# Kernel tuning notes

Measured on AMD Instinct MI355X. Metric: run time of the kernel, lower is better.

The kernel has to match this reference:

```python
import jax, jax.numpy as jnp
import numpy as np

B, IN, K, E = 2048, 1024, 128, 64  # batch, in_features, n_concepts, emb_size


def setup_inputs() -> dict:
    key = jax.random.key(0)
    k1, k2, k3, k4, k5 = jax.random.split(key, 5)
    x = jax.random.normal(k1, (B, IN), dtype=jnp.float32)
    # stacked per-concept Linear(in_features, 2*emb_size)
    W = jax.random.normal(k2, (K, IN, 2 * E), dtype=jnp.float32) * (1.0 / np.sqrt(IN))
    b = jax.random.normal(k3, (K, 2 * E), dtype=jnp.float32) * 0.01
    # shared prob predictor Linear(2*emb_size, 1)
    wp = jax.random.normal(k4, (2 * E,), dtype=jnp.float32) * (1.0 / np.sqrt(2 * E))
    bp = jax.random.normal(k5, (), dtype=jnp.float32) * 0.01
    return {"x": x, "W": W, "b": b, "wp": wp, "bp": bp}


def reference(x, W, b, wp, bp):
    # batched GEMM over all concepts at once: [B,K,2E]
    context = jax.nn.leaky_relu(jnp.einsum('bi,kio->bko', x, W) + b)
    # shared predictor + sigmoid: [B,K]
    c_pred = jax.nn.sigmoid(jnp.einsum('bko,o->bk', context, wp) + bp)
    ctx_pos = context[..., :E]
    ctx_neg = context[..., E:]
    p = c_pred[..., None]
    c_emb = ctx_pos * p + ctx_neg * (1.0 - p)  # [B,K,E]
    return c_emb, c_pred
```

## Files before the change

kernel.cpp:

```cpp
#include <hip/hip_runtime.h>

typedef unsigned int u32;
typedef unsigned short u16;
typedef __attribute__((ext_vector_type(8))) __bf16 bf16x8;
typedef __attribute__((ext_vector_type(4))) float f32x4;

#define B_SZ 2048
#define IN_SZ 1024
#define K_SZ 128
#define E_SZ 64
#define TWOE 128
#define BK 32
static const size_t OUT_EMB = (size_t)B_SZ * K_SZ * E_SZ;

__device__ __forceinline__ u16 f2bf(float f) {
    u32 u = __builtin_bit_cast(u32, f);
    u32 r = u + 0x7fffu + ((u >> 16) & 1u);
    return (u16)(r >> 16);
}

__device__ __forceinline__ void async16(const void* g, void* l) {
    __builtin_amdgcn_global_load_lds((const __attribute__((address_space(1))) u32*)g,
                                     (__attribute__((address_space(3))) u32*)l, 16, 0, 0);
}

__global__ void __launch_bounds__(256) cvt_x(const float* __restrict__ in, u16* __restrict__ outp, int n4) {
    int i = blockIdx.x * blockDim.x + threadIdx.x;
    if (i < n4) {
        float4 v = ((const float4*)in)[i];
        u32 lo = (u32)f2bf(v.x) | ((u32)f2bf(v.y) << 16);
        u32 hi = (u32)f2bf(v.z) | ((u32)f2bf(v.w) << 16);
        ((uint2*)outp)[i] = make_uint2(lo, hi);
    }
}

__global__ void __launch_bounds__(256) cvt_w(const float* __restrict__ W, u16* __restrict__ wt) {
    __shared__ u16 tr[128][72];
    const int k = blockIdx.y, i0 = blockIdx.x * 64;
    const float* src = W + (size_t)k * IN_SZ * TWOE + (size_t)i0 * TWOE;
#pragma unroll
    for (int r = 0; r < 8; ++r) {
        int idx = r * 256 + threadIdx.x;
        int i = idx >> 5;
        int o = (idx & 31) * 4;
        float4 v = ((const float4*)src)[idx];
        tr[o + 0][i] = f2bf(v.x);
        tr[o + 1][i] = f2bf(v.y);
        tr[o + 2][i] = f2bf(v.z);
        tr[o + 3][i] = f2bf(v.w);
    }
    __syncthreads();
    const int o = threadIdx.x >> 1, h = threadIdx.x & 1;
    u16* dst = wt + ((size_t)(k * TWOE + o) * IN_SZ) + i0 + h * 32;
#pragma unroll
    for (int s = 0; s < 4; ++s) {
        uint4 v = *(const uint4*)&tr[o][h * 32 + s * 8];
        ((uint4*)dst)[s] = v;
    }
}

__global__ void __launch_bounds__(256) cvt_pred(const float* __restrict__ pw, float* __restrict__ out) {
    __shared__ float t[128][132];
    const int b0 = blockIdx.x * 128;
    const int tid = threadIdx.x;
#pragma unroll
    for (int i = 0; i < 16; ++i) {
        int idx = i * 256 + tid;
        int kk = idx >> 5, c4 = (idx & 31) * 4;
        float4 v = *(const float4*)(pw + (size_t)kk * B_SZ + b0 + c4);
        t[kk][c4 + 0] = v.x; t[kk][c4 + 1] = v.y; t[kk][c4 + 2] = v.z; t[kk][c4 + 3] = v.w;
    }
    __syncthreads();
#pragma unroll
    for (int i = 0; i < 16; ++i) {
        int idx = i * 256 + tid;
        int bl = idx >> 5, k4 = (idx & 31) * 4;
        float4 v = make_float4(t[k4 + 0][bl], t[k4 + 1][bl], t[k4 + 2][bl], t[k4 + 3][bl]);
        *(float4*)(out + OUT_EMB + (size_t)(b0 + bl) * K_SZ + k4) = v;
    }
}

__global__ void __launch_bounds__(512, 2) fused_main(
    const u16* __restrict__ xb,
    const u16* __restrict__ wt,
    const float* __restrict__ bias, const float* __restrict__ wpv,
    const float* __restrict__ bpp, float* __restrict__ out,
    float* __restrict__ pw) {
    __shared__ union {
        u16 stage[3][20480];
        struct { float pl[512][2]; float ex[256][65]; } epi;
    } sm;

    const int tid = threadIdx.x;
    const int l = tid & 63, w = tid >> 6;
    const int wm = w >> 1, wn = w & 1;
    const int hi = l >> 4, lo16 = l & 15;
    const int q = l >> 2, sl = l & 3;

    const int id = blockIdx.x;
    const int xcd = id & 7, j = id >> 3;
    const int k = (xcd << 4) | (j >> 2);
    const int brow = (j & 3) << 9;

    const u16* abase = xb + (size_t)(brow + w * 16 + q) * IN_SZ + (sl ^ ((q >> 1) & 3)) * 8;
    const u16* bbase = wt + ((size_t)k * TWOE + w * 16 + q) * IN_SZ + (sl ^ ((q >> 1) & 3)) * 8;
    const int aldst = w * 512;
    const int bldst = 16384 + w * 512;

    const int xsl = (hi ^ ((lo16 >> 1) & 3)) << 4;
    const int aoff = (wm * 128 + lo16) * 64 + xsl;
    const int boff = 32768 + (wn * 64 + lo16) * 64 + xsl;

    f32x4 acc[8][4] = {};

    auto STAGE = [&](int bi, int tt) {
        const int koff = tt * BK;
        u16* sbuf = &sm.stage[bi][0];
#pragma unroll
        for (int i = 0; i < 4; ++i)
            async16(abase + (size_t)i * 128 * IN_SZ + koff, sbuf + i * 4096 + aldst);
        async16(bbase + koff, sbuf + bldst);
    };

    const float bp_val = *bpp;
    float bvals[4], wvals[4];
#pragma unroll
    for (int n = 0; n < 4; ++n) {
        const int o = wn * 64 + n * 16 + lo16;
        bvals[n] = bias[k * TWOE + o];
        wvals[n] = wpv[o];
    }

    STAGE(0, 0);
    STAGE(1, 1);
    asm volatile("s_waitcnt vmcnt(5)" ::: "memory");
    __builtin_amdgcn_s_barrier();

    for (int t = 0; t < 32; ++t) {
        const int b0 = t % 3;
        if (t < 30) STAGE((b0 + 2) % 3, t + 2);
        const char* base = (const char*)&sm.stage[b0][0];
        bf16x8 af[8], bfr[4];
#pragma unroll
        for (int m = 0; m < 8; ++m)
            af[m] = *(const bf16x8*)(base + aoff + m * 1024);
#pragma unroll
        for (int n = 0; n < 4; ++n)
            bfr[n] = *(const bf16x8*)(base + boff + n * 1024);
#pragma unroll
        for (int m = 0; m < 8; ++m)
#pragma unroll
            for (int n = 0; n < 4; ++n)
                acc[m][n] = __builtin_amdgcn_mfma_f32_16x16x32_bf16(af[m], bfr[n], acc[m][n], 0, 0, 0);
        if (t < 30) asm volatile("s_waitcnt vmcnt(5) lgkmcnt(0)" ::: "memory");
        else        asm volatile("s_waitcnt vmcnt(0) lgkmcnt(0)" ::: "memory");
        __builtin_amdgcn_s_barrier();
    }

    float p[8][4];
#pragma unroll
    for (int m = 0; m < 8; ++m)
#pragma unroll
        for (int j = 0; j < 4; ++j) {
            float s = 0.f;
#pragma unroll
            for (int n = 0; n < 4; ++n) {
                float v = acc[m][n][j] + bvals[n];
                v = v > 0.f ? v : 0.01f * v;
                acc[m][n][j] = v;
                s += v * wvals[n];
            }
            s += __shfl_xor(s, 1);
            s += __shfl_xor(s, 2);
            s += __shfl_xor(s, 4);
            s += __shfl_xor(s, 8);
            p[m][j] = s;
        }
    if (lo16 == 0) {
#pragma unroll
        for (int m = 0; m < 8; ++m)
#pragma unroll
            for (int j = 0; j < 4; ++j)
                sm.epi.pl[wm * 128 + m * 16 + hi * 4 + j][wn] = p[m][j];
    }
    __builtin_amdgcn_s_barrier();
#pragma unroll
    for (int m = 0; m < 8; ++m)
#pragma unroll
        for (int j = 0; j < 4; ++j) {
            const int rg = wm * 128 + m * 16 + hi * 4 + j;
            const float z = sm.epi.pl[rg][0] + sm.epi.pl[rg][1] + bp_val;
            p[m][j] = 1.f / (1.f + __expf(-z));
        }
    if (wn == 0 && lo16 == 0) {
        if (pw) {
#pragma unroll
            for (int m = 0; m < 8; ++m) {
                float4 v = make_float4(p[m][0], p[m][1], p[m][2], p[m][3]);
                *(float4*)(pw + (size_t)k * B_SZ + brow + wm * 128 + m * 16 + hi * 4) = v;
            }
        } else {
#pragma unroll
            for (int m = 0; m < 8; ++m)
#pragma unroll
                for (int j = 0; j < 4; ++j) {
                    const int b = brow + wm * 128 + m * 16 + hi * 4 + j;
                    out[OUT_EMB + (size_t)b * K_SZ + k] = p[m][j];
                }
        }
    }
#pragma unroll
    for (int h = 0; h < 2; ++h) {
        if (wn == 1) {
#pragma unroll
            for (int mm = 0; mm < 4; ++mm) {
                const int m = h * 4 + mm;
#pragma unroll
                for (int n = 0; n < 4; ++n)
#pragma unroll
                    for (int j = 0; j < 4; ++j)
                        sm.epi.ex[wm * 64 + mm * 16 + hi * 4 + j][n * 16 + lo16] =
                            (1.f - p[m][j]) * acc[m][n][j];
            }
        }
        __builtin_amdgcn_s_barrier();
        if (wn == 0) {
#pragma unroll
            for (int mm = 0; mm < 4; ++mm) {
                const int m = h * 4 + mm;
#pragma unroll
                for (int n = 0; n < 4; ++n)
#pragma unroll
                    for (int j = 0; j < 4; ++j) {
                        const int rl = wm * 64 + mm * 16 + hi * 4 + j;
                        const int b = brow + wm * 128 + m * 16 + hi * 4 + j;
                        const int e = n * 16 + lo16;
                        out[((size_t)b * K_SZ + k) * E_SZ + e] =
                            p[m][j] * acc[m][n][j] + sm.epi.ex[rl][e];
                    }
            }
        }
        __builtin_amdgcn_s_barrier();
    }
}

__global__ void __launch_bounds__(128) fallback_kernel(
    const float* __restrict__ x, const float* __restrict__ W,
    const float* __restrict__ bias, const float* __restrict__ wpv,
    const float* __restrict__ bpp, float* __restrict__ out) {
    const int k = blockIdx.y;
    const int b0 = blockIdx.x * 8;
    const int o = threadIdx.x;
    __shared__ float xs[8][1024];
    __shared__ float red[2];
    __shared__ float exch[64];
    for (int idx = threadIdx.x; idx < 8 * 1024; idx += 128)
        xs[idx >> 10][idx & 1023] = x[(size_t)(b0 + (idx >> 10)) * IN_SZ + (idx & 1023)];
    __syncthreads();
    float a[8] = {};
    for (int i = 0; i < 1024; ++i) {
        float wv = W[((size_t)k * IN_SZ + i) * TWOE + o];
#pragma unroll
        for (int bb = 0; bb < 8; ++bb) a[bb] += xs[bb][i] * wv;
    }
    const float bo = bias[k * TWOE + o], wo = wpv[o], bpv = *bpp;
    for (int bb = 0; bb < 8; ++bb) {
        float c = a[bb] + bo;
        c = c > 0.f ? c : 0.01f * c;
        float s = c * wo;
        for (int off = 1; off < 64; off <<= 1) s += __shfl_xor(s, off);
        if ((threadIdx.x & 63) == 0) red[threadIdx.x >> 6] = s;
        __syncthreads();
        float p = 1.f / (1.f + expf(-(red[0] + red[1] + bpv)));
        if (o >= 64) exch[o - 64] = (1.f - p) * c;
        __syncthreads();
        if (o < 64) out[((size_t)(b0 + bb) * K_SZ + k) * E_SZ + o] = p * c + exch[o];
        if (o == 0) out[OUT_EMB + (size_t)(b0 + bb) * K_SZ + k] = p;
        __syncthreads();
    }
}

extern "C" void kernel_launch(void* const* d_in, const int* in_sizes, int n_in,
                              void* d_out, int out_size, void* d_ws, size_t ws_size,
                              hipStream_t stream) {
    const float* x = (const float*)d_in[0];
    const float* W = (const float*)d_in[1];
    const float* bias = (const float*)d_in[2];
    const float* wp = (const float*)d_in[3];
    const float* bp = (const float*)d_in[4];
    float* out = (float*)d_out;

    const size_t X_ELEMS = (size_t)B_SZ * IN_SZ;
    const size_t WT_ELEMS = (size_t)K_SZ * TWOE * IN_SZ;
    const size_t PW_ELEMS = (size_t)K_SZ * B_SZ;
    const size_t NEED_BASE = (X_ELEMS + WT_ELEMS) * sizeof(u16);
    const size_t NEED_FULL = NEED_BASE + PW_ELEMS * sizeof(float);

    if (ws_size >= NEED_BASE) {
        u16* xb = (u16*)d_ws;
        u16* wt = xb + X_ELEMS;
        float* pw = (ws_size >= NEED_FULL) ? (float*)(wt + WT_ELEMS) : nullptr;
        int n4 = (int)(X_ELEMS / 4);
        cvt_x<<<dim3((n4 + 255) / 256), 256, 0, stream>>>(x, xb, n4);
        cvt_w<<<dim3(16, 128), 256, 0, stream>>>(W, wt);
        fused_main<<<dim3(512), 512, 0, stream>>>(xb, wt, bias, wp, bp, out, pw);
        if (pw) cvt_pred<<<dim3(16), 256, 0, stream>>>(pw, out);
    } else {
        fallback_kernel<<<dim3(B_SZ / 8, K_SZ), 128, 0, stream>>>(x, W, bias, wp, bp, out);
    }
}
```

Baseline: 122.3 us.

## Halve block tile to 256 rows with 4 waves and add MFMA priority

The fused GEMM block now covers 256 batch rows with 256 threads (4 waves) instead of 512 rows with 8 waves, and the grid doubles to 1024 blocks. The staging buffers shrink, the load mapping changes so each wave issues two B-tile async loads, and the wait counts are adjusted to match. The MFMA section is wrapped in s_setprio, and the epilogue drops its two-pass LDS exchange for a single pass. The goal is more blocks per CU and better latency hiding from smaller LDS use, at the cost of reloading each W tile for twice as many blocks.

```diff
diff --git a/kernel.cpp b/kernel.cpp
--- a/kernel.cpp
+++ b/kernel.cpp
@@ -80,15 +80,15 @@
     }
 }
 
-__global__ void __launch_bounds__(512, 2) fused_main(
+__global__ void __launch_bounds__(256, 2) fused_main(
     const u16* __restrict__ xb,
     const u16* __restrict__ wt,
     const float* __restrict__ bias, const float* __restrict__ wpv,
     const float* __restrict__ bpp, float* __restrict__ out,
     float* __restrict__ pw) {
     __shared__ union {
-        u16 stage[3][20480];
-        struct { float pl[512][2]; float ex[256][65]; } epi;
+        u16 stage[3][12288];
+        struct { float pl[256][2]; float ex[256][65]; } epi;
     } sm;
 
     const int tid = threadIdx.x;
@@ -98,18 +98,16 @@
     const int q = l >> 2, sl = l & 3;
 
     const int id = blockIdx.x;
-    const int xcd = id & 7, j = id >> 3;
-    const int k = (xcd << 4) | (j >> 2);
-    const int brow = (j & 3) << 9;
+    const int xcd = id & 7, j2 = id >> 3;
+    const int k = (xcd << 4) | (j2 >> 3);
+    const int brow = (j2 & 7) << 8;
 
     const u16* abase = xb + (size_t)(brow + w * 16 + q) * IN_SZ + (sl ^ ((q >> 1) & 3)) * 8;
     const u16* bbase = wt + ((size_t)k * TWOE + w * 16 + q) * IN_SZ + (sl ^ ((q >> 1) & 3)) * 8;
-    const int aldst = w * 512;
-    const int bldst = 16384 + w * 512;
 
     const int xsl = (hi ^ ((lo16 >> 1) & 3)) << 4;
     const int aoff = (wm * 128 + lo16) * 64 + xsl;
-    const int boff = 32768 + (wn * 64 + lo16) * 64 + xsl;
+    const int boff = 16384 + (wn * 64 + lo16) * 64 + xsl;
 
     f32x4 acc[8][4] = {};
 
@@ -118,8 +116,10 @@
         u16* sbuf = &sm.stage[bi][0];
 #pragma unroll
         for (int i = 0; i < 4; ++i)
-            async16(abase + (size_t)i * 128 * IN_SZ + koff, sbuf + i * 4096 + aldst);
-        async16(bbase + koff, sbuf + bldst);
+            async16(abase + (size_t)i * 64 * IN_SZ + koff, sbuf + i * 2048 + w * 512);
+#pragma unroll
+        for (int jj = 0; jj < 2; ++jj)
+            async16(bbase + (size_t)jj * 64 * IN_SZ + koff, sbuf + 8192 + jj * 2048 + w * 512);
     };
 
     const float bp_val = *bpp;
@@ -133,7 +133,7 @@
 
     STAGE(0, 0);
     STAGE(1, 1);
-    asm volatile("s_waitcnt vmcnt(5)" ::: "memory");
+    asm volatile("s_waitcnt vmcnt(6)" ::: "memory");
     __builtin_amdgcn_s_barrier();
 
     for (int t = 0; t < 32; ++t) {
@@ -147,12 +147,14 @@
 #pragma unroll
         for (int n = 0; n < 4; ++n)
             bfr[n] = *(const bf16x8*)(base + boff + n * 1024);
+        __builtin_amdgcn_s_setprio(1);
 #pragma unroll
         for (int m = 0; m < 8; ++m)
 #pragma unroll
             for (int n = 0; n < 4; ++n)
                 acc[m][n] = __builtin_amdgcn_mfma_f32_16x16x32_bf16(af[m], bfr[n], acc[m][n], 0, 0, 0);
-        if (t < 30) asm volatile("s_waitcnt vmcnt(5) lgkmcnt(0)" ::: "memory");
+        __builtin_amdgcn_s_setprio(0);
+        if (t < 30) asm volatile("s_waitcnt vmcnt(6) lgkmcnt(0)" ::: "memory");
         else        asm volatile("s_waitcnt vmcnt(0) lgkmcnt(0)" ::: "memory");
         __builtin_amdgcn_s_barrier();
     }
@@ -209,38 +211,30 @@
                 }
         }
     }
-#pragma unroll
-    for (int h = 0; h < 2; ++h) {
-        if (wn == 1) {
-#pragma unroll
-            for (int mm = 0; mm < 4; ++mm) {
-                const int m = h * 4 + mm;
-#pragma unroll
-                for (int n = 0; n < 4; ++n)
-#pragma unroll
-                    for (int j = 0; j < 4; ++j)
-                        sm.epi.ex[wm * 64 + mm * 16 + hi * 4 + j][n * 16 + lo16] =
-                            (1.f - p[m][j]) * acc[m][n][j];
-            }
-        }
-        __builtin_amdgcn_s_barrier();
-        if (wn == 0) {
-#pragma unroll
-            for (int mm = 0; mm < 4; ++mm) {
-                const int m = h * 4 + mm;
-#pragma unroll
-                for (int n = 0; n < 4; ++n)
-#pragma unroll
-                    for (int j = 0; j < 4; ++j) {
-                        const int rl = wm * 64 + mm * 16 + hi * 4 + j;
-                        const int b = brow + wm * 128 + m * 16 + hi * 4 + j;
-                        const int e = n * 16 + lo16;
-                        out[((size_t)b * K_SZ + k) * E_SZ + e] =
-                            p[m][j] * acc[m][n][j] + sm.epi.ex[rl][e];
-                    }
-            }
-        }
-        __builtin_amdgcn_s_barrier();
+    if (wn == 1) {
+#pragma unroll
+        for (int m = 0; m < 8; ++m)
+#pragma unroll
+            for (int n = 0; n < 4; ++n)
+#pragma unroll
+                for (int j = 0; j < 4; ++j)
+                    sm.epi.ex[wm * 128 + m * 16 + hi * 4 + j][n * 16 + lo16] =
+                        (1.f - p[m][j]) * acc[m][n][j];
+    }
+    __builtin_amdgcn_s_barrier();
+    if (wn == 0) {
+#pragma unroll
+        for (int m = 0; m < 8; ++m)
+#pragma unroll
+            for (int n = 0; n < 4; ++n)
+#pragma unroll
+                for (int j = 0; j < 4; ++j) {
+                    const int rl = wm * 128 + m * 16 + hi * 4 + j;
+                    const int b = brow + rl;
+                    const int e = n * 16 + lo16;
+                    out[((size_t)b * K_SZ + k) * E_SZ + e] =
+                        p[m][j] * acc[m][n][j] + sm.epi.ex[rl][e];
+                }
     }
 }
 
@@ -303,7 +297,7 @@
         int n4 = (int)(X_ELEMS / 4);
         cvt_x<<<dim3((n4 + 255) / 256), 256, 0, stream>>>(x, xb, n4);
         cvt_w<<<dim3(16, 128), 256, 0, stream>>>(W, wt);
-        fused_main<<<dim3(512), 512, 0, stream>>>(xb, wt, bias, wp, bp, out, pw);
+        fused_main<<<dim3(1024), 256, 0, stream>>>(xb, wt, bias, wp, bp, out, pw);
         if (pw) cvt_pred<<<dim3(16), 256, 0, stream>>>(pw, out);
     } else {
         fallback_kernel<<<dim3(B_SZ / 8, K_SZ), 128, 0, stream>>>(x, W, bias, wp, bp, out);
```

Result: faster. 119.8 us (-2.1%).
